# Optimization experiments

Measured on AMD Instinct MI355X. Metric: run time of the kernel, lower is better.

The kernel has to match this reference:

```python
import jax, jax.numpy as jnp
import numpy as np

N_NODES = 100000
N_EDGES = 1600000
IN_DIM = 128
HID_DIM = 64


def setup_inputs() -> dict:
    key = jax.random.key(0)
    ks = jax.random.split(key, 8)
    feat = jax.random.normal(ks[0], (N_NODES, IN_DIM), dtype=jnp.float32)
    # xavier-normal-like scaling for gcn weights
    w1 = jax.random.normal(ks[1], (IN_DIM, HID_DIM), dtype=jnp.float32) * np.sqrt(2.0 / (IN_DIM + HID_DIM))
    w2 = jax.random.normal(ks[2], (HID_DIM, HID_DIM), dtype=jnp.float32) * np.sqrt(2.0 / (HID_DIM + HID_DIM))
    conv_w = jax.random.normal(ks[3], (2, 1, 3), dtype=jnp.float32) * np.sqrt(2.0 / 3.0)
    conv_b = jax.random.uniform(ks[4], (2,), dtype=jnp.float32, minval=-1.0 / np.sqrt(3.0), maxval=1.0 / np.sqrt(3.0))
    ref_radius = jnp.zeros((1,), dtype=jnp.float32)
    src = jax.random.randint(ks[5], (N_EDGES,), 0, N_NODES, dtype=jnp.int32)
    dst = jax.random.randint(ks[6], (N_EDGES,), 0, N_NODES, dtype=jnp.int32)
    return {"feat": feat, "w1": w1, "w2": w2, "conv_w": conv_w, "conv_b": conv_b,
            "ref_radius": ref_radius, "src": src, "dst": dst}


def _dropout(h, key, p=0.5):
    keep = jax.random.bernoulli(key, 1.0 - p, h.shape)
    return jnp.where(keep, h / (1.0 - p), 0.0)


def _gcn(h, w, norm, src2, dst2, n, pre_matmul):
    # norm-scale -> (matmul) -> copy_src/sum scatter -> (matmul) -> norm-scale -> relu
    h = h * norm[:, None]
    if pre_matmul:  # in_feats > out_feats branch
        h = h @ w
        agg = jax.ops.segment_sum(h[src2], dst2, num_segments=n)
    else:
        agg = jax.ops.segment_sum(h[src2], dst2, num_segments=n)
        agg = agg @ w
    rst = agg * norm[:, None]
    return jax.nn.relu(rst)


def reference(feat, w1, w2, conv_w, conv_b, ref_radius, src, dst):
    n = feat.shape[0]
    # dgl.add_self_loop
    loops = jnp.arange(n, dtype=src.dtype)
    src2 = jnp.concatenate([src, loops])
    dst2 = jnp.concatenate([dst, loops])
    deg = jax.ops.segment_sum(jnp.ones_like(dst2, dtype=jnp.float32), dst2, num_segments=n)
    norm = jnp.clip(deg, 1.0, None) ** -0.5  # [n]

    dkey = jax.random.key(42)
    k1, k2 = jax.random.split(dkey)

    h = _gcn(feat, w1, norm, src2, dst2, n, pre_matmul=True)   # 128 > 64
    h = _dropout(h, k1)
    h = _gcn(h, w2, norm, src2, dst2, n, pre_matmul=False)     # 64 == 64
    h = _dropout(h, k2)

    # conv1d: [n, hid] -> [n, 1, hid] -> [n, 2, hid-2] -> [n, 2*(hid-2)]
    x = h[:, None, :]
    y = jax.lax.conv_general_dilated(x, conv_w, window_strides=(1,), padding='VALID',
                                     dimension_numbers=('NCH', 'OIH', 'NCH'))
    y = y + conv_b[None, :, None]
    h = y.reshape(n, -1)

    # hypersphere: distance of each node feature from the centroid vs ref radius
    o = jnp.mean(h, axis=0)
    radius = jnp.sqrt(jnp.sum((h - o + 1e-6) ** 2, axis=1))  # F.pairwise_distance eps=1e-6
    dis = jnp.clip(radius - ref_radius, 1e-4, 1.0 - 1e-4)
    return dis, ref_radius
```

## Files before the change

### kernel.cpp

```cpp
#include <hip/hip_runtime.h>
#include <stdint.h>

#define HID 64
#define INDIM 128
#define NBK 512
#define NBLK 512
#define EPBCAP 3200
#define BK3CAP 8192
#define CSREP 32

typedef __attribute__((ext_vector_type(8))) short bf16x8;
typedef __attribute__((ext_vector_type(4))) float f32x4;
typedef __attribute__((ext_vector_type(2))) float f32x2;

__host__ __device__ __forceinline__ void tf2x32(uint32_t k0, uint32_t k1,
                                                uint32_t x0, uint32_t x1,
                                                uint32_t& o0, uint32_t& o1) {
  uint32_t ks2 = k0 ^ k1 ^ 0x1BD11BDAu;
#define ROTL(v, r) (((v) << (r)) | ((v) >> (32 - (r))))
#define RND(r) { x0 += x1; x1 = ROTL(x1, r); x1 ^= x0; }
  x0 += k0; x1 += k1;
  RND(13) RND(15) RND(26) RND(6)
  x0 += k1; x1 += ks2 + 1u;
  RND(17) RND(29) RND(16) RND(24)
  x0 += ks2; x1 += k0 + 2u;
  RND(13) RND(15) RND(26) RND(6)
  x0 += k0; x1 += k1 + 3u;
  RND(17) RND(29) RND(16) RND(24)
  x0 += k1; x1 += ks2 + 4u;
  RND(13) RND(15) RND(26) RND(6)
  x0 += ks2; x1 += k0 + 5u;
  o0 = x0; o1 = x1;
#undef RND
#undef ROTL
}

__device__ __forceinline__ float tf_uniform(uint32_t ka, uint32_t kb, uint32_t j) {
  uint32_t o0, o1;
  tf2x32(ka, kb, 0u, j, o0, o1);
  uint32_t bits = o0 ^ o1;
  uint32_t f = (bits >> 9) | 0x3f800000u;
  return __uint_as_float(f) - 1.0f;
}

__device__ __forceinline__ unsigned short f2bf(float f) {
  uint32_t x = __float_as_uint(f);
  uint32_t r = (x + 0x7fffu + ((x >> 16) & 1u)) >> 16;
  return (unsigned short)r;
}

__device__ __forceinline__ float bf2f_lo(uint32_t u) { return __uint_as_float(u << 16); }
__device__ __forceinline__ float bf2f_hi(uint32_t u) { return __uint_as_float(u & 0xffff0000u); }

__device__ __forceinline__ unsigned char f2fp8(float v) {
  return (unsigned char)(__builtin_amdgcn_cvt_pk_fp8_f32(v, 0.f, 0, false) & 0xff);
}

__global__ __launch_bounds__(256) void binsort_k(const int* __restrict__ src,
                                                 const int* __restrict__ dst,
                                                 uint32_t* __restrict__ sorted,
                                                 int* __restrict__ blockoff2,
                                                 const float* __restrict__ w1,
                                                 const float* __restrict__ w2,
                                                 unsigned short* __restrict__ w1t,
                                                 unsigned short* __restrict__ w2t,
                                                 float* __restrict__ colsumR,
                                                 int E, int EPB, int NB) {
  __shared__ uint32_t lbuf[EPBCAP];
  __shared__ int dbuf[EPBCAP];
  __shared__ int ha[NBK], hb[NBK], cursor[NBK];
  int b = blockIdx.x, t = threadIdx.x;
  {
    int i = b * 256 + t;
    if (i < CSREP * HID) colsumR[i] = 0.f;
    if (i < INDIM * HID) {
      int c = i >> 7, k = i & 127;
      w1t[i] = f2bf(w1[k * HID + c]);
    } else if (i < INDIM * HID + HID * HID) {
      int j = i - INDIM * HID;
      int c = j >> 6, k = j & 63;
      w2t[j] = f2bf(w2[k * HID + c]);
    }
  }
  int e0 = b * EPB;
  int e1 = e0 + EPB; if (e1 > E) e1 = E;
  int m = e1 - e0;
  ha[t] = 0; ha[t + 256] = 0;
  __syncthreads();
  for (int i = t; i < m; i += 256) {
    int d = dst[e0 + i];
    dbuf[i] = d;
    atomicAdd(&ha[d >> 8], 1);
  }
  __syncthreads();
  int* cur = ha; int* nxt = hb;
  for (int off = 1; off < 512; off <<= 1) {
    int i0 = t, i1 = t + 256;
    int v0 = cur[i0] + ((i0 >= off) ? cur[i0 - off] : 0);
    int v1 = cur[i1] + ((i1 >= off) ? cur[i1 - off] : 0);
    __syncthreads();
    nxt[i0] = v0; nxt[i1] = v1;
    __syncthreads();
    int* tmp = cur; cur = nxt; nxt = tmp;
  }
  for (int i = t; i < NB; i += 256) {
    int ex = (i == 0) ? 0 : cur[i - 1];
    cursor[i] = ex;
    blockoff2[(size_t)i * NBLK + b] = ex;
  }
  if (t == 0) blockoff2[(size_t)NB * NBLK + b] = m;
  __syncthreads();
  for (int i = t; i < m; i += 256) {
    int d = dbuf[i], s = src[e0 + i];
    int pos = atomicAdd(&cursor[d >> 8], 1);
    lbuf[pos] = ((uint32_t)s << 8) | (uint32_t)(d & 255);
  }
  __syncthreads();
  for (int i = t; i < m; i += 256) sorted[e0 + i] = lbuf[i];
}

__global__ __launch_bounds__(256) void csrbuild_k(const uint32_t* __restrict__ sorted,
                                                  const int* __restrict__ blockoff2,
                                                  int* __restrict__ rowstart,
                                                  int* __restrict__ csr,
                                                  float* __restrict__ norm,
                                                  int NB, int n, int E, int EPB) {
  __shared__ uint32_t ebuf[BK3CAP];
  __shared__ int sa[256], sb[256], cursor[256];
  __shared__ int sc_[NBLK], sd_[NBLK];
  int bid = blockIdx.x, t = threadIdx.x;
  int xcd = bid & 7, sub = bid >> 3;
  int qq = NB >> 3, rr = NB & 7;
  int k = (xcd < rr ? xcd * (qq + 1) : rr * (qq + 1) + (xcd - rr) * qq) + sub;

  int b0 = t, b1 = t + 256;
  int lo0 = blockoff2[(size_t)k * NBLK + b0];
  int lo1 = blockoff2[(size_t)k * NBLK + b1];
  int hi0 = blockoff2[(size_t)(k + 1) * NBLK + b0];
  int hi1 = blockoff2[(size_t)(k + 1) * NBLK + b1];
  int len0 = hi0 - lo0, len1 = hi1 - lo1;
  sa[t] = lo0 + lo1;
  sc_[b0] = len0; sc_[b1] = len1;
  __syncthreads();
  for (int off = 128; off > 0; off >>= 1) {
    if (t < off) sa[t] += sa[t + off];
    __syncthreads();
  }
  int s0 = sa[0];
  int* cur = sc_; int* nxt = sd_;
  for (int off = 1; off < NBLK; off <<= 1) {
    int v0 = cur[b0] + ((b0 >= off) ? cur[b0 - off] : 0);
    int v1 = cur[b1] + ((b1 >= off) ? cur[b1 - off] : 0);
    __syncthreads();
    nxt[b0] = v0; nxt[b1] = v1;
    __syncthreads();
    int* tmp = cur; cur = nxt; nxt = tmp;
  }
  int M = cur[NBLK - 1];
  int dd0 = cur[b0] - len0, dd1 = cur[b1] - len1;
  {
    const uint32_t* sp = sorted + (size_t)b0 * EPB;
    for (int i = lo0; i < hi0; i++) ebuf[dd0 + (i - lo0)] = sp[i];
  }
  {
    const uint32_t* sp = sorted + (size_t)b1 * EPB;
    for (int i = lo1; i < hi1; i++) ebuf[dd1 + (i - lo1)] = sp[i];
  }
  cursor[t] = 0;
  __syncthreads();
  for (int i = t; i < M; i += 256) atomicAdd(&cursor[ebuf[i] & 255], 1);
  __syncthreads();
  int cnt = cursor[t];
  sa[t] = cnt;
  int* cu2 = sa; int* nx2 = sb;
  __syncthreads();
  for (int off = 1; off < 256; off <<= 1) {
    int v = cu2[t] + ((t >= off) ? cu2[t - off] : 0);
    __syncthreads();
    nx2[t] = v;
    __syncthreads();
    int* tmp = cu2; cu2 = nx2; nx2 = tmp;
  }
  int localrow = cu2[t] - cnt;
  int node = k * 256 + t;
  if (node < n) {
    rowstart[node] = s0 + localrow;
    norm[node] = rsqrtf((float)(cnt + 1));
  }
  if (k == NB - 1 && t == 255) rowstart[n] = E;
  cursor[t] = localrow;
  __syncthreads();
  for (int i = t; i < M; i += 256) {
    uint32_t pe = ebuf[i];
    int pos = atomicAdd(&cursor[pe & 255], 1);
    csr[s0 + pos] = (int)(pe >> 8);
  }
}

__global__ __launch_bounds__(256) void gemm1(const float* __restrict__ feat,
                                             const unsigned short* __restrict__ w1t,
                                             const float* __restrict__ norm,
                                             unsigned char* __restrict__ h0, int n) {
  int t = threadIdx.x;
  int wv = t >> 6, lane = t & 63;
  int strip = blockIdx.x * 4 + wv;
  if (strip * 16 >= n) return;
  int m = lane & 15, q = lane >> 4;
  bf16x8 Bf[4][4];
#pragma unroll
  for (int kc = 0; kc < 4; kc++)
#pragma unroll
    for (int ct = 0; ct < 4; ct++)
      Bf[kc][ct] = *(const bf16x8*)(w1t + (ct * 16 + m) * INDIM + kc * 32 + q * 8);
  const float* arow = feat + (size_t)(strip * 16 + m) * INDIM;
  bf16x8 Af[4];
#pragma unroll
  for (int kc = 0; kc < 4; kc++) {
    const float* pa = arow + kc * 32 + q * 8;
    bf16x8 a;
#pragma unroll
    for (int j = 0; j < 8; j++) a[j] = (short)f2bf(pa[j]);
    Af[kc] = a;
  }
  f32x4 acc[4] = {{0.f,0.f,0.f,0.f},{0.f,0.f,0.f,0.f},{0.f,0.f,0.f,0.f},{0.f,0.f,0.f,0.f}};
#pragma unroll
  for (int kc = 0; kc < 4; kc++)
#pragma unroll
    for (int ct = 0; ct < 4; ct++)
      acc[ct] = __builtin_amdgcn_mfma_f32_16x16x32_bf16(Af[kc], Bf[kc][ct], acc[ct], 0, 0, 0);
#pragma unroll
  for (int r = 0; r < 4; r++) {
    int row = strip * 16 + q * 4 + r;
    float nm = norm[row];
#pragma unroll
    for (int ct = 0; ct < 4; ct++)
      h0[(size_t)row * HID + ct * 16 + m] = f2fp8(acc[ct][r] * nm);
  }
}

__global__ __launch_bounds__(256) void gather_k(const uint32_t* __restrict__ h8,
                                                uint32_t* __restrict__ outp,
                                                const int* __restrict__ rowstart,
                                                const int* __restrict__ csr,
                                                const float* __restrict__ norm,
                                                int n, uint32_t ka, uint32_t kb) {
  int wid = (int)((blockIdx.x * 256u + threadIdx.x) >> 6);
  int d0 = wid * 4;
  if (d0 >= n) return;
  int lane = threadIdx.x & 63;
  int g = lane >> 4, c4 = lane & 15;
  int g4 = g << 2;

  int rr = d0 + (lane < 4 ? lane : 4);
  if (rr > n) rr = n;
  int rsl = rowstart[rr];
  int r0[5];
#pragma unroll
  for (int i = 0; i < 5; ++i) r0[i] = __shfl(rsl, i);
  int L[4];
#pragma unroll
  for (int i = 0; i < 4; ++i) L[i] = r0[i + 1] - r0[i];

  int selfrow = d0 + g; if (selfrow >= n) selfrow = d0;
  uint32_t uself = h8[(size_t)selfrow * 16 + c4];

  int idx[4];
#pragma unroll
  for (int i = 0; i < 4; ++i) {
    int la = L[i] < 32 ? L[i] : 32;
    idx[i] = (lane < la) ? csr[r0[i] + lane] : 0;
  }

  uint32_t u[4][8];
#pragma unroll
  for (int i = 0; i < 4; ++i) {
#pragma unroll
    for (int t = 0; t < 8; ++t) {
      int s = __builtin_amdgcn_ds_bpermute(16 * t + g4, idx[i]);
      u[i][t] = (4 * t + g < L[i]) ? h8[(size_t)(uint32_t)s * 16 + c4] : 0u;
    }
  }

  f32x2 al[4], ah[4];
#pragma unroll
  for (int i = 0; i < 4; ++i) { al[i] = (f32x2){0.f, 0.f}; ah[i] = (f32x2){0.f, 0.f}; }
#pragma unroll
  for (int i = 0; i < 4; ++i) {
#pragma unroll
    for (int t = 0; t < 8; ++t) {
      al[i] += __builtin_amdgcn_cvt_pk_f32_fp8((int)u[i][t], false);
      ah[i] += __builtin_amdgcn_cvt_pk_f32_fp8((int)u[i][t], true);
    }
  }

#pragma unroll
  for (int i = 0; i < 4; ++i) {
    if (L[i] > 32) {
      for (int e0 = 32; e0 < L[i]; e0 += 4) {
        int e = e0 + g;
        uint32_t uu = 0u;
        if (e < L[i]) {
          int s = csr[r0[i] + e];
          uu = h8[(size_t)(uint32_t)s * 16 + c4];
        }
        al[i] += __builtin_amdgcn_cvt_pk_f32_fp8((int)uu, false);
        ah[i] += __builtin_amdgcn_cvt_pk_f32_fp8((int)uu, true);
      }
    }
  }

  f32x2 sl, sh, rl2, rh2;
  sl = (g & 1) ? al[0] : al[1];
  sh = (g & 1) ? ah[0] : ah[1];
  rl2.x = __shfl_xor(sl.x, 16); rl2.y = __shfl_xor(sl.y, 16);
  rh2.x = __shfl_xor(sh.x, 16); rh2.y = __shfl_xor(sh.y, 16);
  f32x2 fABl = ((g & 1) ? al[1] : al[0]) + rl2;
  f32x2 fABh = ((g & 1) ? ah[1] : ah[0]) + rh2;
  sl = (g & 1) ? al[2] : al[3];
  sh = (g & 1) ? ah[2] : ah[3];
  rl2.x = __shfl_xor(sl.x, 16); rl2.y = __shfl_xor(sl.y, 16);
  rh2.x = __shfl_xor(sh.x, 16); rh2.y = __shfl_xor(sh.y, 16);
  f32x2 fCDl = ((g & 1) ? al[3] : al[2]) + rl2;
  f32x2 fCDh = ((g & 1) ? ah[3] : ah[2]) + rh2;
  sl = (g & 2) ? fABl : fCDl;
  sh = (g & 2) ? fABh : fCDh;
  rl2.x = __shfl_xor(sl.x, 32); rl2.y = __shfl_xor(sl.y, 32);
  rh2.x = __shfl_xor(sh.x, 32); rh2.y = __shfl_xor(sh.y, 32);
  f32x2 tl = ((g & 2) ? fCDl : fABl) + rl2;
  f32x2 th = ((g & 2) ? fCDh : fABh) + rh2;

  tl += __builtin_amdgcn_cvt_pk_f32_fp8((int)uself, false);
  th += __builtin_amdgcn_cvt_pk_f32_fp8((int)uself, true);

  int d = d0 + g;
  uint32_t jb = (uint32_t)d0 * 64u + (uint32_t)lane;
  float u0 = tf_uniform(ka, kb, jb);
  float u1 = tf_uniform(ka, kb, jb + 64u);
  float u2 = tf_uniform(ka, kb, jb + 128u);
  float u3 = tf_uniform(ka, kb, jb + 192u);
  unsigned long long kp0 = __ballot(u0 < 0.5f);
  unsigned long long kp1 = __ballot(u1 < 0.5f);
  unsigned long long kp2 = __ballot(u2 < 0.5f);
  unsigned long long kp3 = __ballot(u3 < 0.5f);
  unsigned long long keep = (g & 2) ? ((g & 1) ? kp3 : kp2)
                                    : ((g & 1) ? kp1 : kp0);
  uint32_t kb4 = (uint32_t)(keep >> (4 * c4)) & 15u;
  float nm = norm[d < n ? d : d0];
  float v0 = fmaxf(tl.x * nm, 0.f), v1 = fmaxf(tl.y * nm, 0.f);
  float v2 = fmaxf(th.x * nm, 0.f), v3 = fmaxf(th.y * nm, 0.f);
  float s2 = 2.f * nm;
  v0 = (kb4 & 1u) ? v0 * s2 : 0.f;
  v1 = (kb4 & 2u) ? v1 * s2 : 0.f;
  v2 = (kb4 & 4u) ? v2 * s2 : 0.f;
  v3 = (kb4 & 8u) ? v3 * s2 : 0.f;
  if (d < n) {
    int o = __builtin_amdgcn_cvt_pk_fp8_f32(v0, v1, 0, false);
    o = __builtin_amdgcn_cvt_pk_fp8_f32(v2, v3, o, true);
    outp[(size_t)d * 16 + c4] = (uint32_t)o;
  }
}

__global__ __launch_bounds__(256) void gather2gemm2_k(
    const uint32_t* __restrict__ h8, const int* __restrict__ rowstart,
    const int* __restrict__ csr, const float* __restrict__ norm,
    const unsigned short* __restrict__ w2t, unsigned short* __restrict__ h2,
    float* __restrict__ colsumR, int n, uint32_t ka, uint32_t kb) {
  __shared__ unsigned short abuf[16][72];
  int t = threadIdx.x;
  int wv = t >> 6, lane = t & 63;
  int node0 = blockIdx.x * 16;
  int d0 = node0 + wv * 4;
  int g = lane >> 4, c4 = lane & 15;
  int g4 = g << 2;
  int lrow = (wv << 2) + g;

  if (d0 < n) {
    int rr = d0 + (lane < 4 ? lane : 4);
    if (rr > n) rr = n;
    int rsl = rowstart[rr];
    int r0[5];
#pragma unroll
    for (int i = 0; i < 5; ++i) r0[i] = __shfl(rsl, i);
    int L[4];
#pragma unroll
    for (int i = 0; i < 4; ++i) L[i] = r0[i + 1] - r0[i];

    int selfrow = d0 + g; if (selfrow >= n) selfrow = d0;
    uint32_t uself = h8[(size_t)selfrow * 16 + c4];

    int idx[4];
#pragma unroll
    for (int i = 0; i < 4; ++i) {
      int la = L[i] < 32 ? L[i] : 32;
      idx[i] = (lane < la) ? csr[r0[i] + lane] : 0;
    }

    uint32_t u[4][8];
#pragma unroll
    for (int i = 0; i < 4; ++i) {
#pragma unroll
      for (int tt = 0; tt < 8; ++tt) {
        int s = __builtin_amdgcn_ds_bpermute(16 * tt + g4, idx[i]);
        u[i][tt] = (4 * tt + g < L[i]) ? h8[(size_t)(uint32_t)s * 16 + c4] : 0u;
      }
    }

    f32x2 al[4], ah[4];
#pragma unroll
    for (int i = 0; i < 4; ++i) { al[i] = (f32x2){0.f, 0.f}; ah[i] = (f32x2){0.f, 0.f}; }
#pragma unroll
    for (int i = 0; i < 4; ++i) {
#pragma unroll
      for (int tt = 0; tt < 8; ++tt) {
        al[i] += __builtin_amdgcn_cvt_pk_f32_fp8((int)u[i][tt], false);
        ah[i] += __builtin_amdgcn_cvt_pk_f32_fp8((int)u[i][tt], true);
      }
    }

#pragma unroll
    for (int i = 0; i < 4; ++i) {
      if (L[i] > 32) {
        for (int e0 = 32; e0 < L[i]; e0 += 4) {
          int e = e0 + g;
          uint32_t uu = 0u;
          if (e < L[i]) {
            int s = csr[r0[i] + e];
            uu = h8[(size_t)(uint32_t)s * 16 + c4];
          }
          al[i] += __builtin_amdgcn_cvt_pk_f32_fp8((int)uu, false);
          ah[i] += __builtin_amdgcn_cvt_pk_f32_fp8((int)uu, true);
        }
      }
    }

    f32x2 sl, sh, rl2, rh2;
    sl = (g & 1) ? al[0] : al[1];
    sh = (g & 1) ? ah[0] : ah[1];
    rl2.x = __shfl_xor(sl.x, 16); rl2.y = __shfl_xor(sl.y, 16);
    rh2.x = __shfl_xor(sh.x, 16); rh2.y = __shfl_xor(sh.y, 16);
    f32x2 fABl = ((g & 1) ? al[1] : al[0]) + rl2;
    f32x2 fABh = ((g & 1) ? ah[1] : ah[0]) + rh2;
    sl = (g & 1) ? al[2] : al[3];
    sh = (g & 1) ? ah[2] : ah[3];
    rl2.x = __shfl_xor(sl.x, 16); rl2.y = __shfl_xor(sl.y, 16);
    rh2.x = __shfl_xor(sh.x, 16); rh2.y = __shfl_xor(sh.y, 16);
    f32x2 fCDl = ((g & 1) ? al[3] : al[2]) + rl2;
    f32x2 fCDh = ((g & 1) ? ah[3] : ah[2]) + rh2;
    sl = (g & 2) ? fABl : fCDl;
    sh = (g & 2) ? fABh : fCDh;
    rl2.x = __shfl_xor(sl.x, 32); rl2.y = __shfl_xor(sl.y, 32);
    rh2.x = __shfl_xor(sh.x, 32); rh2.y = __shfl_xor(sh.y, 32);
    f32x2 tl = ((g & 2) ? fCDl : fABl) + rl2;
    f32x2 th = ((g & 2) ? fCDh : fABh) + rh2;

    tl += __builtin_amdgcn_cvt_pk_f32_fp8((int)uself, false);
    th += __builtin_amdgcn_cvt_pk_f32_fp8((int)uself, true);

    uint2 w;
    w.x = (uint32_t)f2bf(tl.x) | ((uint32_t)f2bf(tl.y) << 16);
    w.y = (uint32_t)f2bf(th.x) | ((uint32_t)f2bf(th.y) << 16);
    if (d0 + g >= n) { w.x = 0u; w.y = 0u; }
    *(uint2*)&abuf[lrow][4 * c4] = w;
  } else {
    uint2 z; z.x = 0u; z.y = 0u;
    *(uint2*)&abuf[lrow][4 * c4] = z;
  }
  __syncthreads();
  if (wv != 0) return;
  if (node0 >= n) return;

  int m = lane & 15, q = lane >> 4;
  f32x4 acc[4] = {{0.f,0.f,0.f,0.f},{0.f,0.f,0.f,0.f},{0.f,0.f,0.f,0.f},{0.f,0.f,0.f,0.f}};
#pragma unroll
  for (int kc = 0; kc < 2; kc++) {
    bf16x8 Af = *(const bf16x8*)&abuf[m][kc * 32 + q * 8];
#pragma unroll
    for (int ct = 0; ct < 4; ct++) {
      bf16x8 Bf = *(const bf16x8*)(w2t + (ct * 16 + m) * HID + kc * 32 + q * 8);
      acc[ct] = __builtin_amdgcn_mfma_f32_16x16x32_bf16(Af, Bf, acc[ct], 0, 0, 0);
    }
  }
  float cs[4] = {0.f, 0.f, 0.f, 0.f};
#pragma unroll
  for (int r = 0; r < 4; r++) {
    int row = node0 + q * 4 + r;
    if (row < n) {
      float nm = norm[row];
#pragma unroll
      for (int ct = 0; ct < 4; ct++) {
        int col = ct * 16 + m;
        float v = fmaxf(acc[ct][r] * nm, 0.f);
        float uu = tf_uniform(ka, kb, (uint32_t)row * 64u + (uint32_t)col);
        v = (uu < 0.5f) ? v * 2.f : 0.f;
        h2[(size_t)row * HID + col] = f2bf(v);
        cs[ct] += v;
      }
    }
  }
#pragma unroll
  for (int ct = 0; ct < 4; ct++) {
    cs[ct] += __shfl_xor(cs[ct], 16);
    cs[ct] += __shfl_xor(cs[ct], 32);
  }
  if (q == 0) {
    float* dstc = colsumR + (blockIdx.x & (CSREP - 1)) * HID;
#pragma unroll
    for (int ct = 0; ct < 4; ct++) atomicAdd(&dstc[ct * 16 + m], cs[ct]);
  }
}

__global__ __launch_bounds__(128) void final_k(const uint32_t* __restrict__ h2u,
                                               const float* __restrict__ colsumR,
                                               const float* __restrict__ conv_w,
                                               const float* __restrict__ conv_b,
                                               const float* __restrict__ ref_radius,
                                               float* __restrict__ out, int n) {
  __shared__ float rows[128 * 67];
  __shared__ float omean[124];
  __shared__ float cm[HID];
  int t = threadIdx.x;
  int node0 = blockIdx.x * 128;
  if (t < HID) {
    float s = 0.f;
#pragma unroll
    for (int r = 0; r < CSREP; r++) s += colsumR[r * HID + t];
    cm[t] = s * (1.0f / (float)n);
  }
  for (int idx = t; idx < 128 * 32; idx += 128) {
    int r = idx >> 5, cpi = idx & 31;
    int node = node0 + r;
    uint32_t u = (node < n) ? h2u[(size_t)node * 32 + cpi] : 0u;
    rows[r * 67 + 2 * cpi] = bf2f_lo(u);
    rows[r * 67 + 2 * cpi + 1] = bf2f_hi(u);
  }
  __syncthreads();
  if (t < 124) {
    int o = t / 62, i = t % 62;
    omean[t] = conv_b[o] + conv_w[o * 3] * cm[i] + conv_w[o * 3 + 1] * cm[i + 1] +
               conv_w[o * 3 + 2] * cm[i + 2];
  }
  __syncthreads();
  int node = node0 + t;
  if (node < n) {
    float r0[HID];
#pragma unroll
    for (int k = 0; k < HID; k++) r0[k] = rows[t * 67 + k];
    float w00 = conv_w[0], w01 = conv_w[1], w02 = conv_w[2];
    float w10 = conv_w[3], w11 = conv_w[4], w12 = conv_w[5];
    float b0 = conv_b[0], b1 = conv_b[1];
    float acc = 0.f;
#pragma unroll
    for (int i = 0; i < 62; i++) {
      float y0 = b0 + w00 * r0[i] + w01 * r0[i + 1] + w02 * r0[i + 2];
      float d0 = y0 - omean[i] + 1e-6f;
      acc += d0 * d0;
      float y1 = b1 + w10 * r0[i] + w11 * r0[i + 1] + w12 * r0[i + 2];
      float d1 = y1 - omean[62 + i] + 1e-6f;
      acc += d1 * d1;
    }
    float radius = sqrtf(acc);
    float dis = fminf(fmaxf(radius - ref_radius[0], 1e-4f), 1.f - 1e-4f);
    out[node] = dis;
  }
  if (blockIdx.x == 0 && t == 0) out[n] = ref_radius[0];
}

extern "C" void kernel_launch(void* const* d_in, const int* in_sizes, int n_in,
                              void* d_out, int out_size, void* d_ws, size_t ws_size,
                              hipStream_t stream) {
  const float* feat = (const float*)d_in[0];
  const float* w1 = (const float*)d_in[1];
  const float* w2 = (const float*)d_in[2];
  const float* conv_w = (const float*)d_in[3];
  const float* conv_b = (const float*)d_in[4];
  const float* ref_radius = (const float*)d_in[5];
  const int* src = (const int*)d_in[6];
  const int* dst = (const int*)d_in[7];
  int n = in_sizes[0] / INDIM;
  int E = in_sizes[6];
  float* out = (float*)d_out;

  int NB = (n + 255) >> 8;
  int EPB = (E + NBLK - 1) / NBLK;

  char* p = (char*)d_ws;
  auto carve = [&](size_t bytes) { void* r = (void*)p; p += (bytes + 255) & ~(size_t)255; return r; };
  float* norm = (float*)carve((size_t)n * 4);
  float* colsumR = (float*)carve((size_t)CSREP * HID * 4);
  int* rowstart = (int*)carve(((size_t)n + 1) * 4);
  int* blockoff2 = (int*)carve((size_t)(NB + 1) * NBLK * 4);
  uint32_t* sorted = (uint32_t*)carve((size_t)E * 4);
  int* csr = (int*)carve((size_t)E * 4);
  unsigned short* w1t = (unsigned short*)carve((size_t)INDIM * HID * 2);
  unsigned short* w2t = (unsigned short*)carve((size_t)HID * HID * 2);
  unsigned char* H0f8 = (unsigned char*)carve((size_t)n * HID);
  unsigned char* Tf8 = (unsigned char*)carve((size_t)n * HID);
  unsigned short* H2bf = (unsigned short*)carve((size_t)n * HID * 2);

  uint32_t k1a, k1b, k2a, k2b;
  tf2x32(0u, 42u, 0u, 0u, k1a, k1b);
  tf2x32(0u, 42u, 0u, 1u, k2a, k2b);

  int gatherB = (n + 15) / 16;
  int stripB = ((n + 15) / 16 + 3) / 4;

  binsort_k<<<NBLK, 256, 0, stream>>>(src, dst, sorted, blockoff2, w1, w2, w1t, w2t, colsumR, E, EPB, NB);
  csrbuild_k<<<NB, 256, 0, stream>>>(sorted, blockoff2, rowstart, csr, norm, NB, n, E, EPB);
  gemm1<<<stripB, 256, 0, stream>>>(feat, w1t, norm, H0f8, n);
  gather_k<<<gatherB, 256, 0, stream>>>((const uint32_t*)H0f8, (uint32_t*)Tf8, rowstart, csr, norm, n, k1a, k1b);
  gather2gemm2_k<<<gatherB, 256, 0, stream>>>((const uint32_t*)Tf8, rowstart, csr, norm, w2t, H2bf, colsumR, n, k2a, k2b);
  final_k<<<(n + 127) / 128, 128, 0, stream>>>((const uint32_t*)H2bf, colsumR, conv_w, conv_b, ref_radius, out, n);
}
```

Baseline: 233.3 us.

## Replace LDS bin-sort CSR build with global atomic counting sort

Replaces the two-kernel block-local bucket sort with a simpler CSR construction: a global degree histogram via atomics, a two-level prefix scan, and an atomic scatter of source indices into CSR slots. The aim is to remove the heavy shared-memory sorting passes and the serial per-thread copy loops in the old build. In exchange it adds more launches plus a memset, random global atomics, and uncoalesced scatter writes, and edge order within rows becomes nondeterministic.

```diff
diff --git a/kernel.cpp b/kernel.cpp
--- a/kernel.cpp
+++ b/kernel.cpp
@@ -3,10 +3,6 @@
 
 #define HID 64
 #define INDIM 128
-#define NBK 512
-#define NBLK 512
-#define EPBCAP 3200
-#define BK3CAP 8192
 #define CSREP 32
 
 typedef __attribute__((ext_vector_type(8))) short bf16x8;
@@ -56,144 +52,85 @@
   return (unsigned char)(__builtin_amdgcn_cvt_pk_fp8_f32(v, 0.f, 0, false) & 0xff);
 }
 
-__global__ __launch_bounds__(256) void binsort_k(const int* __restrict__ src,
-                                                 const int* __restrict__ dst,
-                                                 uint32_t* __restrict__ sorted,
-                                                 int* __restrict__ blockoff2,
-                                                 const float* __restrict__ w1,
-                                                 const float* __restrict__ w2,
-                                                 unsigned short* __restrict__ w1t,
-                                                 unsigned short* __restrict__ w2t,
-                                                 float* __restrict__ colsumR,
-                                                 int E, int EPB, int NB) {
-  __shared__ uint32_t lbuf[EPBCAP];
-  __shared__ int dbuf[EPBCAP];
-  __shared__ int ha[NBK], hb[NBK], cursor[NBK];
+__global__ __launch_bounds__(256) void hist_k(const int* __restrict__ dst,
+                                              int* __restrict__ deg,
+                                              const float* __restrict__ w1,
+                                              const float* __restrict__ w2,
+                                              unsigned short* __restrict__ w1t,
+                                              unsigned short* __restrict__ w2t,
+                                              float* __restrict__ colsumR, int E) {
+  int i = blockIdx.x * 256 + threadIdx.x;
+  if (i < CSREP * HID) colsumR[i] = 0.f;
+  if (i < INDIM * HID) {
+    int c = i >> 7, k = i & 127;
+    w1t[i] = f2bf(w1[k * HID + c]);
+  } else if (i < INDIM * HID + HID * HID) {
+    int j = i - INDIM * HID;
+    int c = j >> 6, k = j & 63;
+    w2t[j] = f2bf(w2[k * HID + c]);
+  }
+  if (i < E) atomicAdd(&deg[dst[i]], 1);
+}
+
+__global__ __launch_bounds__(256) void scan1_k(const int* __restrict__ deg,
+                                               int* __restrict__ scn,
+                                               int* __restrict__ btot, int n) {
+  __shared__ int sa[256], sb[256];
   int b = blockIdx.x, t = threadIdx.x;
-  {
-    int i = b * 256 + t;
-    if (i < CSREP * HID) colsumR[i] = 0.f;
-    if (i < INDIM * HID) {
-      int c = i >> 7, k = i & 127;
-      w1t[i] = f2bf(w1[k * HID + c]);
-    } else if (i < INDIM * HID + HID * HID) {
-      int j = i - INDIM * HID;
-      int c = j >> 6, k = j & 63;
-      w2t[j] = f2bf(w2[k * HID + c]);
-    }
-  }
-  int e0 = b * EPB;
-  int e1 = e0 + EPB; if (e1 > E) e1 = E;
-  int m = e1 - e0;
-  ha[t] = 0; ha[t + 256] = 0;
+  int node = b * 256 + t;
+  int v = (node < n) ? deg[node] : 0;
+  sa[t] = v;
   __syncthreads();
-  for (int i = t; i < m; i += 256) {
-    int d = dst[e0 + i];
-    dbuf[i] = d;
-    atomicAdd(&ha[d >> 8], 1);
-  }
-  __syncthreads();
-  int* cur = ha; int* nxt = hb;
-  for (int off = 1; off < 512; off <<= 1) {
-    int i0 = t, i1 = t + 256;
-    int v0 = cur[i0] + ((i0 >= off) ? cur[i0 - off] : 0);
-    int v1 = cur[i1] + ((i1 >= off) ? cur[i1 - off] : 0);
+  int* cur = sa; int* nxt = sb;
+  for (int off = 1; off < 256; off <<= 1) {
+    int x = cur[t] + ((t >= off) ? cur[t - off] : 0);
     __syncthreads();
-    nxt[i0] = v0; nxt[i1] = v1;
+    nxt[t] = x;
     __syncthreads();
     int* tmp = cur; cur = nxt; nxt = tmp;
   }
-  for (int i = t; i < NB; i += 256) {
-    int ex = (i == 0) ? 0 : cur[i - 1];
-    cursor[i] = ex;
-    blockoff2[(size_t)i * NBLK + b] = ex;
-  }
-  if (t == 0) blockoff2[(size_t)NB * NBLK + b] = m;
-  __syncthreads();
-  for (int i = t; i < m; i += 256) {
-    int d = dbuf[i], s = src[e0 + i];
-    int pos = atomicAdd(&cursor[d >> 8], 1);
-    lbuf[pos] = ((uint32_t)s << 8) | (uint32_t)(d & 255);
-  }
-  __syncthreads();
-  for (int i = t; i < m; i += 256) sorted[e0 + i] = lbuf[i];
-}
-
-__global__ __launch_bounds__(256) void csrbuild_k(const uint32_t* __restrict__ sorted,
-                                                  const int* __restrict__ blockoff2,
-                                                  int* __restrict__ rowstart,
-                                                  int* __restrict__ csr,
-                                                  float* __restrict__ norm,
-                                                  int NB, int n, int E, int EPB) {
-  __shared__ uint32_t ebuf[BK3CAP];
-  __shared__ int sa[256], sb[256], cursor[256];
-  __shared__ int sc_[NBLK], sd_[NBLK];
-  int bid = blockIdx.x, t = threadIdx.x;
-  int xcd = bid & 7, sub = bid >> 3;
-  int qq = NB >> 3, rr = NB & 7;
-  int k = (xcd < rr ? xcd * (qq + 1) : rr * (qq + 1) + (xcd - rr) * qq) + sub;
-
-  int b0 = t, b1 = t + 256;
-  int lo0 = blockoff2[(size_t)k * NBLK + b0];
-  int lo1 = blockoff2[(size_t)k * NBLK + b1];
-  int hi0 = blockoff2[(size_t)(k + 1) * NBLK + b0];
-  int hi1 = blockoff2[(size_t)(k + 1) * NBLK + b1];
-  int len0 = hi0 - lo0, len1 = hi1 - lo1;
-  sa[t] = lo0 + lo1;
-  sc_[b0] = len0; sc_[b1] = len1;
+  if (node < n) scn[node] = cur[t];
+  if (t == 255) btot[b] = cur[255];
+}
+
+__global__ __launch_bounds__(256) void scan2_k(const int* __restrict__ scn,
+                                               const int* __restrict__ btot,
+                                               const int* __restrict__ deg,
+                                               int* __restrict__ rowstart,
+                                               int* __restrict__ cursor,
+                                               float* __restrict__ norm,
+                                               int n, int E) {
+  __shared__ int red[256];
+  int b = blockIdx.x, t = threadIdx.x;
+  int acc = 0;
+  for (int i = t; i < b; i += 256) acc += btot[i];
+  red[t] = acc;
   __syncthreads();
   for (int off = 128; off > 0; off >>= 1) {
-    if (t < off) sa[t] += sa[t + off];
+    if (t < off) red[t] += red[t + off];
     __syncthreads();
   }
-  int s0 = sa[0];
-  int* cur = sc_; int* nxt = sd_;
-  for (int off = 1; off < NBLK; off <<= 1) {
-    int v0 = cur[b0] + ((b0 >= off) ? cur[b0 - off] : 0);
-    int v1 = cur[b1] + ((b1 >= off) ? cur[b1 - off] : 0);
-    __syncthreads();
-    nxt[b0] = v0; nxt[b1] = v1;
-    __syncthreads();
-    int* tmp = cur; cur = nxt; nxt = tmp;
-  }
-  int M = cur[NBLK - 1];
-  int dd0 = cur[b0] - len0, dd1 = cur[b1] - len1;
-  {
-    const uint32_t* sp = sorted + (size_t)b0 * EPB;
-    for (int i = lo0; i < hi0; i++) ebuf[dd0 + (i - lo0)] = sp[i];
-  }
-  {
-    const uint32_t* sp = sorted + (size_t)b1 * EPB;
-    for (int i = lo1; i < hi1; i++) ebuf[dd1 + (i - lo1)] = sp[i];
-  }
-  cursor[t] = 0;
-  __syncthreads();
-  for (int i = t; i < M; i += 256) atomicAdd(&cursor[ebuf[i] & 255], 1);
-  __syncthreads();
-  int cnt = cursor[t];
-  sa[t] = cnt;
-  int* cu2 = sa; int* nx2 = sb;
-  __syncthreads();
-  for (int off = 1; off < 256; off <<= 1) {
-    int v = cu2[t] + ((t >= off) ? cu2[t - off] : 0);
-    __syncthreads();
-    nx2[t] = v;
-    __syncthreads();
-    int* tmp = cu2; cu2 = nx2; nx2 = tmp;
-  }
-  int localrow = cu2[t] - cnt;
-  int node = k * 256 + t;
+  int off0 = red[0];
+  int node = b * 256 + t;
   if (node < n) {
-    rowstart[node] = s0 + localrow;
+    int cnt = deg[node];
+    int rs = off0 + scn[node] - cnt;
+    rowstart[node] = rs;
+    cursor[node] = rs;
     norm[node] = rsqrtf((float)(cnt + 1));
   }
-  if (k == NB - 1 && t == 255) rowstart[n] = E;
-  cursor[t] = localrow;
-  __syncthreads();
-  for (int i = t; i < M; i += 256) {
-    uint32_t pe = ebuf[i];
-    int pos = atomicAdd(&cursor[pe & 255], 1);
-    csr[s0 + pos] = (int)(pe >> 8);
+  if (b == 0 && t == 0) rowstart[n] = E;
+}
+
+__global__ __launch_bounds__(256) void scat_k(const int* __restrict__ src,
+                                              const int* __restrict__ dst,
+                                              int* __restrict__ cursor,
+                                              int* __restrict__ csr, int E) {
+  int i = blockIdx.x * 256 + threadIdx.x;
+  if (i < E) {
+    int d = dst[i], s = src[i];
+    int pos = atomicAdd(&cursor[d], 1);
+    csr[pos] = s;
   }
 }
 
@@ -581,15 +518,16 @@
   float* out = (float*)d_out;
 
   int NB = (n + 255) >> 8;
-  int EPB = (E + NBLK - 1) / NBLK;
 
   char* p = (char*)d_ws;
   auto carve = [&](size_t bytes) { void* r = (void*)p; p += (bytes + 255) & ~(size_t)255; return r; };
   float* norm = (float*)carve((size_t)n * 4);
   float* colsumR = (float*)carve((size_t)CSREP * HID * 4);
   int* rowstart = (int*)carve(((size_t)n + 1) * 4);
-  int* blockoff2 = (int*)carve((size_t)(NB + 1) * NBLK * 4);
-  uint32_t* sorted = (uint32_t*)carve((size_t)E * 4);
+  int* deg = (int*)carve((size_t)n * 4);
+  int* scn = (int*)carve((size_t)n * 4);
+  int* btot = (int*)carve((size_t)NB * 4);
+  int* cursor = (int*)carve((size_t)n * 4);
   int* csr = (int*)carve((size_t)E * 4);
   unsigned short* w1t = (unsigned short*)carve((size_t)INDIM * HID * 2);
   unsigned short* w2t = (unsigned short*)carve((size_t)HID * HID * 2);
@@ -601,11 +539,15 @@
   tf2x32(0u, 42u, 0u, 0u, k1a, k1b);
   tf2x32(0u, 42u, 0u, 1u, k2a, k2b);
 
+  int edgeB = (E + 255) / 256;
   int gatherB = (n + 15) / 16;
   int stripB = ((n + 15) / 16 + 3) / 4;
 
-  binsort_k<<<NBLK, 256, 0, stream>>>(src, dst, sorted, blockoff2, w1, w2, w1t, w2t, colsumR, E, EPB, NB);
-  csrbuild_k<<<NB, 256, 0, stream>>>(sorted, blockoff2, rowstart, csr, norm, NB, n, E, EPB);
+  hipMemsetAsync(deg, 0, (size_t)n * 4, stream);
+  hist_k<<<edgeB, 256, 0, stream>>>(dst, deg, w1, w2, w1t, w2t, colsumR, E);
+  scan1_k<<<NB, 256, 0, stream>>>(deg, scn, btot, n);
+  scan2_k<<<NB, 256, 0, stream>>>(scn, btot, deg, rowstart, cursor, norm, n, E);
+  scat_k<<<edgeB, 256, 0, stream>>>(src, dst, cursor, csr, E);
   gemm1<<<stripB, 256, 0, stream>>>(feat, w1t, norm, H0f8, n);
   gather_k<<<gatherB, 256, 0, stream>>>((const uint32_t*)H0f8, (uint32_t*)Tf8, rowstart, csr, norm, n, k1a, k1b);
   gather2gemm2_k<<<gatherB, 256, 0, stream>>>((const uint32_t*)Tf8, rowstart, csr, norm, w2t, H2bf, colsumR, n, k2a, k2b);
```

New measurement: 403.6 us. 1.73x slower.
